# Performance work log

Measured on AMD Instinct MI355X. Metric: run time of the kernel, lower is better.

The kernel has to match this reference:

```python
import jax, jax.numpy as jnp
import numpy as np

N, F, HID, H, B = 400000, 128, 32, 4, 2000

def setup_inputs() -> dict:
    key = jax.random.key(0)
    ks = jax.random.split(key, 8)
    atom_fea = jax.random.normal(ks[0], (N, F), dtype=jnp.float32)
    segment_ids = jnp.sort(jax.random.randint(ks[1], (N,), 0, B, dtype=jnp.int32))
    s = 0.05
    return {
        "atom_fea": atom_fea,
        "segment_ids": segment_ids,
        "num_crystals": B,
        "W1": jax.random.normal(ks[2], (F, HID), dtype=jnp.float32) * s,
        "b1": jnp.zeros((HID,), dtype=jnp.float32),
        "W2": jax.random.normal(ks[3], (HID, H), dtype=jnp.float32) * s,
        "b2": jnp.zeros((H,), dtype=jnp.float32),
        "Wp": jax.random.normal(ks[4], (H * F, F), dtype=jnp.float32) * s,
        "bp": jnp.zeros((F,), dtype=jnp.float32),
    }

def reference(atom_fea, segment_ids, num_crystals, W1, b1, W2, b2, Wp, bp):
    # key MLP: (N,F) -> (N,H) attention logits (dropout is eval no-op)
    logits = jax.nn.silu(atom_fea @ W1 + b1) @ W2 + b2  # (N,H)
    # segment softmax over atoms within each crystal, per head
    seg_max = jax.ops.segment_max(logits, segment_ids, num_segments=num_crystals)
    ex = jnp.exp(logits - seg_max[segment_ids])
    denom = jax.ops.segment_sum(ex, segment_ids, num_segments=num_crystals)
    w = ex / denom[segment_ids]  # (N,H)
    # per-head softmax-weighted segment sum of atom features -> (B,H,F)
    weighted = jax.ops.segment_sum(
        w[:, :, None] * atom_fea[:, None, :], segment_ids, num_segments=num_crystals
    )
    flat = weighted.reshape(num_crystals, -1)  # (B, H*F)
    return jax.nn.silu(flat @ Wp + bp)  # (B,F)
```

## Files before the change

### kernel.cpp

```cpp
#include <hip/hip_runtime.h>
#include <math.h>

#define F 128
#define HID 32
#define NH 4
#define TILE 32
#define ROWB 512

typedef __attribute__((ext_vector_type(8))) short bf16x8;
typedef __attribute__((ext_vector_type(4))) float f32x4;

__device__ __forceinline__ float silu_f(float x) {
    return x / (1.0f + __expf(-x));
}

__device__ __forceinline__ uint f2bf(float f) {
    union { float f; uint u; } v; v.f = f;
    uint r = v.u + 0x7fffu + ((v.u >> 16) & 1u);
    return r >> 16;
}

__device__ __forceinline__ uint cvtpk_bf16(float lo, float hi) {
    uint r;
    asm("v_cvt_pk_bf16_f32 %0, %1, %2" : "=v"(r) : "v"(lo), "v"(hi));
    return r;
}

__device__ __forceinline__ void gload_lds16(const void* g, void* l) {
    __builtin_amdgcn_global_load_lds(
        (const __attribute__((address_space(1))) void*)g,
        (__attribute__((address_space(3))) void*)l, 16, 0, 0);
}

__global__ void seg_starts_kernel(const int* __restrict__ seg, int* __restrict__ starts,
                                  int N, int B) {
    int i = blockIdx.x * blockDim.x + threadIdx.x;
    if (i >= N) return;
    int id = seg[i];
    if (i == 0) {
        for (int b = 0; b <= id; ++b) starts[b] = 0;
    } else {
        int prev = seg[i - 1];
        for (int b = prev + 1; b <= id; ++b) starts[b] = i;
    }
    if (i == N - 1) {
        for (int b = id + 1; b <= B; ++b) starts[b] = N;
    }
}

__global__ __launch_bounds__(256, 4) void fused16_kernel(
    const float* __restrict__ atom_fea, const int* __restrict__ starts,
    const float* __restrict__ W1, const float* __restrict__ b1,
    const float* __restrict__ W2, const float* __restrict__ b2,
    const float* __restrict__ Wp, const float* __restrict__ bp,
    float* __restrict__ out) {
    __shared__ float sStage[2][TILE * F];
    __shared__ float sP[2 * TILE * 5];
    __shared__ float sTW[NH * 65];

    const int t = threadIdx.x;
    const int b = blockIdx.x;
    const int start = starts[b];
    const int end = starts[b + 1];
    const int wv = t >> 6;
    const int lane = t & 63;
    const int lg = lane >> 4;
    const int l15 = lane & 15;
    const int ag = wv & 1;
    const int mh = wv >> 1;
    const int ca = lane & 3;
    const int co = (lane >> 2) & 15;

    int roff[4], coff[4];
    #pragma unroll
    for (int i = 0; i < 4; ++i) {
        const int q = i * 256 + t;
        roff[i] = q >> 5;
        coff[i] = ((q & 31) ^ (roff[i] & 7)) << 4;
    }

    bf16x8 w1f[4];
    #pragma unroll
    for (int kk = 0; kk < 4; ++kk) {
        bf16x8 fr;
        #pragma unroll
        for (int j = 0; j < 8; ++j)
            fr[j] = (short)f2bf(W1[(kk * 32 + lg * 8 + j) * HID + mh * 16 + l15]);
        w1f[kk] = fr;
    }
    float b1r[4], w2r[4][4];
    #pragma unroll
    for (int r = 0; r < 4; ++r) {
        const int h = mh * 16 + lg * 4 + r;
        b1r[r] = b1[h];
        #pragma unroll
        for (int j = 0; j < 4; ++j) w2r[r][j] = W2[h * NH + j];
    }
    const float b2w = b2[wv];

    float m_run = -INFINITY;
    float s_part = 0.0f;
    float acc8[8] = {0, 0, 0, 0, 0, 0, 0, 0};

    const int nt = (end > start) ? (end - start + TILE - 1) / TILE : 0;
    const char* gbase = (const char*)atom_fea;

    if (nt > 0) {
        #pragma unroll
        for (int i = 0; i < 4; ++i) {
            int a = start + roff[i]; a = (a < end) ? a : end - 1;
            gload_lds16(gbase + (size_t)a * ROWB + coff[i],
                        (char*)sStage[0] + i * 4096 + wv * 1024);
        }
    }
    __syncthreads();

    int pb = 0;
    for (int ti = 0; ti < nt; ++ti) {
        const int base = start + ti * TILE;
        const int T = min(TILE, end - base);
        const char* bufc = (const char*)sStage[pb];
        const bool has_next = (ti + 1 < nt);

        if (has_next) {
            const int nbase = base + TILE;
            char* ldst = (char*)sStage[pb ^ 1];
            #pragma unroll
            for (int i = 0; i < 4; ++i) {
                int a = nbase + roff[i]; a = (a < end) ? a : end - 1;
                gload_lds16(gbase + (size_t)a * ROWB + coff[i],
                            ldst + i * 4096 + wv * 1024);
            }
        }

        {
            f32x4 acc;
            #pragma unroll
            for (int r = 0; r < 4; ++r) acc[r] = b1r[r];
            const int row = ag * 16 + l15;
            const char* rb = bufc + row * ROWB;
            const int rs = row & 7;
            #pragma unroll
            for (int kk = 0; kk < 4; ++kk) {
                const int c0 = kk * 8 + lg * 2;
                const float4 va = *(const float4*)(rb + ((c0 ^ rs) << 4));
                const float4 vb = *(const float4*)(rb + (((c0 + 1) ^ rs) << 4));
                union { bf16x8 v; uint u[4]; } fr;
                fr.u[0] = cvtpk_bf16(va.x, va.y);
                fr.u[1] = cvtpk_bf16(va.z, va.w);
                fr.u[2] = cvtpk_bf16(vb.x, vb.y);
                fr.u[3] = cvtpk_bf16(vb.z, vb.w);
                acc = __builtin_amdgcn_mfma_f32_16x16x32_bf16(w1f[kk], fr.v, acc, 0, 0, 0);
            }
            float p0 = 0, p1 = 0, p2 = 0, p3 = 0;
            #pragma unroll
            for (int r = 0; r < 4; ++r) {
                const float s = silu_f(acc[r]);
                p0 = fmaf(s, w2r[r][0], p0);
                p1 = fmaf(s, w2r[r][1], p1);
                p2 = fmaf(s, w2r[r][2], p2);
                p3 = fmaf(s, w2r[r][3], p3);
            }
            p0 += __shfl_xor(p0, 16); p0 += __shfl_xor(p0, 32);
            p1 += __shfl_xor(p1, 16); p1 += __shfl_xor(p1, 32);
            p2 += __shfl_xor(p2, 16); p2 += __shfl_xor(p2, 32);
            p3 += __shfl_xor(p3, 16); p3 += __shfl_xor(p3, 32);
            if (lane < 16) {
                float* d = &sP[(mh * TILE + ag * 16 + lane) * 5];
                d[0] = p0; d[1] = p1; d[2] = p2; d[3] = p3;
            }
        }
        asm volatile("s_waitcnt lgkmcnt(0)" ::: "memory");
        __builtin_amdgcn_s_barrier();

        {
            const float v = (lane < T)
                ? sP[lane * 5 + wv] + sP[(TILE + lane) * 5 + wv] + b2w
                : -INFINITY;
            if (__any(v > m_run + 8.0f)) {
                float mt = v;
                #pragma unroll
                for (int d = 1; d < 64; d <<= 1) mt = fmaxf(mt, __shfl_xor(mt, d));
                const float m_new = fmaxf(m_run, mt);
                const float r = __expf(m_run - m_new);
                s_part *= r;
                #pragma unroll
                for (int j = 0; j < 8; ++j) acc8[j] *= r;
                m_run = m_new;
            }
            const float e = (lane < T) ? __expf(v - m_run) : 0.0f;
            sTW[wv * 65 + lane] = e;
            s_part += e;
        }

        {
            #pragma unroll 4
            for (int i = 0; i < 8; ++i) {
                const int a = i * 4 + ca;
                const float w = sTW[wv * 65 + a];
                const int sw = a & 7;
                const char* ra = bufc + a * ROWB;
                const float4 v0 = *(const float4*)(ra + (((2 * co) ^ sw) << 4));
                const float4 v1 = *(const float4*)(ra + (((2 * co + 1) ^ sw) << 4));
                acc8[0] = fmaf(w, v0.x, acc8[0]);
                acc8[1] = fmaf(w, v0.y, acc8[1]);
                acc8[2] = fmaf(w, v0.z, acc8[2]);
                acc8[3] = fmaf(w, v0.w, acc8[3]);
                acc8[4] = fmaf(w, v1.x, acc8[4]);
                acc8[5] = fmaf(w, v1.y, acc8[5]);
                acc8[6] = fmaf(w, v1.z, acc8[6]);
                acc8[7] = fmaf(w, v1.w, acc8[7]);
            }
        }
        __syncthreads();
        pb ^= 1;
    }

    #pragma unroll
    for (int d = 1; d < 64; d <<= 1) s_part += __shfl_xor(s_part, d);
    const float inv = (s_part > 0.0f) ? 1.0f / s_part : 0.0f;
    #pragma unroll
    for (int j = 0; j < 8; ++j) {
        acc8[j] += __shfl_xor(acc8[j], 1);
        acc8[j] += __shfl_xor(acc8[j], 2);
    }
    float* sWacc = (float*)sStage;
    float* sPart = (float*)sStage + 512;
    if ((lane & 3) == 0) {
        float* dst = &sWacc[wv * F + (lane >> 2) * 8];
        dst[0] = acc8[0] * inv; dst[1] = acc8[1] * inv;
        dst[2] = acc8[2] * inv; dst[3] = acc8[3] * inv;
        dst[4] = acc8[4] * inv; dst[5] = acc8[5] * inv;
        dst[6] = acc8[6] * inv; dst[7] = acc8[7] * inv;
    }
    __syncthreads();

    {
        const int f = t & 127, half = t >> 7;
        float sum = 0.0f;
        const float* wp = Wp + (size_t)(half * 256) * F + f;
        const float* wa = &sWacc[half * 256];
        for (int k0 = 0; k0 < 256; k0 += 8) {
            float wpv[8];
            #pragma unroll
            for (int u = 0; u < 8; ++u) wpv[u] = wp[(size_t)(k0 + u) * F];
            #pragma unroll
            for (int u = 0; u < 8; ++u) sum = fmaf(wa[k0 + u], wpv[u], sum);
        }
        sPart[t] = sum;
    }
    __syncthreads();
    if (t < 128) out[(size_t)b * F + t] = silu_f(sPart[t] + sPart[t + 128] + bp[t]);
}

extern "C" void kernel_launch(void* const* d_in, const int* in_sizes, int n_in,
                              void* d_out, int out_size, void* d_ws, size_t ws_size,
                              hipStream_t stream) {
    const float* atom_fea = (const float*)d_in[0];
    const int* seg = (const int*)d_in[1];
    const float* W1 = (const float*)d_in[3];
    const float* b1 = (const float*)d_in[4];
    const float* W2 = (const float*)d_in[5];
    const float* b2 = (const float*)d_in[6];
    const float* Wp = (const float*)d_in[7];
    const float* bp = (const float*)d_in[8];
    float* out = (float*)d_out;

    const int N = in_sizes[0] / F;
    const int B = out_size / F;
    int* starts = (int*)d_ws;

    seg_starts_kernel<<<(N + 255) / 256, 256, 0, stream>>>(seg, starts, N, B);
    fused16_kernel<<<B, 256, 0, stream>>>(atom_fea, starts, W1, b1, W2, b2, Wp, bp, out);
}
```

Baseline: 62.31 us.

## Replace segment-starts kernel with in-kernel wave-parallel binary search

Drops the separate seg_starts kernel launch and its workspace. Each wave of the fused kernel now finds its crystal's start and end with a 64-way ballot-based search over the sorted segment ids. This removes one launch and a dependent kernel boundary, at the cost of a few serialized global-load rounds (about three per bound for N=400k) at the start of every block.

Result: no change. 61.66 us (median of 2 runs) (-1.0%).

```diff
diff --git a/kernel.cpp b/kernel.cpp
--- a/kernel.cpp
+++ b/kernel.cpp
@@ -32,24 +32,30 @@
         (__attribute__((address_space(3))) void*)l, 16, 0, 0);
 }
 
-__global__ void seg_starts_kernel(const int* __restrict__ seg, int* __restrict__ starts,
-                                  int N, int B) {
-    int i = blockIdx.x * blockDim.x + threadIdx.x;
-    if (i >= N) return;
-    int id = seg[i];
-    if (i == 0) {
-        for (int b = 0; b <= id; ++b) starts[b] = 0;
-    } else {
-        int prev = seg[i - 1];
-        for (int b = prev + 1; b <= id; ++b) starts[b] = i;
-    }
-    if (i == N - 1) {
-        for (int b = id + 1; b <= B; ++b) starts[b] = N;
-    }
-}
-
-__global__ __launch_bounds__(256, 4) void fused16_kernel(
-    const float* __restrict__ atom_fea, const int* __restrict__ starts,
+__device__ __forceinline__ int lower_bound_wave(const int* __restrict__ seg, int N,
+                                                int v, int lane) {
+    int lo = 0, hi = N;
+    while (hi - lo > 64) {
+        const int step = ((hi - lo) + 63) >> 6;
+        const int idx = lo + lane * step;
+        const bool inr = (idx < hi);
+        const int val = inr ? seg[idx] : 0;
+        const unsigned long long m = __ballot(inr && (val < v));
+        const int cnt = __popcll(m);
+        if (cnt == 0) return lo;
+        const int probe_hi = lo + cnt * step;
+        lo = lo + (cnt - 1) * step + 1;
+        hi = (probe_hi < hi) ? probe_hi : hi;
+    }
+    const int idx = lo + lane;
+    const bool inr = (idx < hi);
+    const int val = inr ? seg[idx] : 0;
+    const unsigned long long m = __ballot(inr && (val < v));
+    return lo + __popcll(m);
+}
+
+__global__ __launch_bounds__(256, 4) void fused17_kernel(
+    const float* __restrict__ atom_fea, const int* __restrict__ seg, int N,
     const float* __restrict__ W1, const float* __restrict__ b1,
     const float* __restrict__ W2, const float* __restrict__ b2,
     const float* __restrict__ Wp, const float* __restrict__ bp,
@@ -60,8 +66,6 @@
 
     const int t = threadIdx.x;
     const int b = blockIdx.x;
-    const int start = starts[b];
-    const int end = starts[b + 1];
     const int wv = t >> 6;
     const int lane = t & 63;
     const int lg = lane >> 4;
@@ -70,6 +74,9 @@
     const int mh = wv >> 1;
     const int ca = lane & 3;
     const int co = (lane >> 2) & 15;
+
+    const int start = lower_bound_wave(seg, N, b, lane);
+    const int end = lower_bound_wave(seg, N, b + 1, lane);
 
     int roff[4], coff[4];
     #pragma unroll
@@ -268,8 +275,6 @@
 
     const int N = in_sizes[0] / F;
     const int B = out_size / F;
-    int* starts = (int*)d_ws;
-
-    seg_starts_kernel<<<(N + 255) / 256, 256, 0, stream>>>(seg, starts, N, B);
-    fused16_kernel<<<B, 256, 0, stream>>>(atom_fea, starts, W1, b1, W2, b2, Wp, bp, out);
-}
+
+    fused17_kernel<<<B, 256, 0, stream>>>(atom_fea, seg, N, W1, b1, W2, b2, Wp, bp, out);
+}
```
